# Kernel optimization log

Measured on AMD Instinct MI355X. Metric: run time of the kernel, lower is better.

The kernel has to match this reference:

```python
import jax, jax.numpy as jnp
import numpy as np

H = 1024      # hidden_size
NH = 16       # num heads
HD = H // NH  # head dim
B, S = 2, 2048


def setup_inputs() -> dict:
    key = jax.random.key(0)
    ks = jax.random.split(key, 10)
    s = 1.0 / np.sqrt(H)
    return {
        "hidden_states": jax.random.normal(ks[0], (B, S, H), dtype=jnp.float32),
        "attention_mask": jax.random.randint(ks[1], (B, S), 0, 2, dtype=jnp.int32),
        "Wq": jax.random.normal(ks[2], (H, H), dtype=jnp.float32) * s,
        "bq": jnp.zeros((H,), dtype=jnp.float32),
        "Wk": jax.random.normal(ks[3], (H, H), dtype=jnp.float32) * s,
        "bk": jnp.zeros((H,), dtype=jnp.float32),
        "Wv": jax.random.normal(ks[4], (H, H), dtype=jnp.float32) * s,
        "bv": jnp.zeros((H,), dtype=jnp.float32),
        "Wo": jax.random.normal(ks[5], (H, H), dtype=jnp.float32) * s,
        "bo": jnp.zeros((H,), dtype=jnp.float32),
    }


def _heads(x):
    # [B,S,H] -> [B,NH,S,HD]
    b, s, _ = x.shape
    return x.reshape(b, s, NH, HD).transpose(0, 2, 1, 3)


def reference(hidden_states, attention_mask, Wq, bq, Wk, bk, Wv, bv, Wo, bo):
    q = _heads(hidden_states @ Wq + bq)
    k = _heads(hidden_states @ Wk + bk)
    v = _heads(hidden_states @ Wv + bv)
    scores = jnp.einsum("bhqd,bhkd->bhqk", q, k) / jnp.sqrt(jnp.float32(HD))
    mask = attention_mask.astype(scores.dtype)[:, None, None, :]  # [B,1,1,S]
    scores = scores + mask * -10000.0
    probs = jax.nn.softmax(scores, axis=-1)  # dropout is identity in eval
    ctx = jnp.einsum("bhqk,bhkd->bhqd", probs, v)
    ctx = ctx.transpose(0, 2, 1, 3).reshape(hidden_states.shape[0], hidden_states.shape[1], H)
    return ctx @ Wo + bo
```

## Files before the change

kernel.cpp:

```cpp
#include <hip/hip_runtime.h>
#include <stdint.h>
#include <stddef.h>

#define S_LEN 2048
#define BATCH 2
#define HID 1024
#define NHEADS 16
#define HDIM 64

typedef __attribute__((ext_vector_type(8))) short short8;
typedef __attribute__((ext_vector_type(4))) short short4v;
typedef __attribute__((ext_vector_type(4))) float float4v;

#define MFMA32(a, b, c) __builtin_amdgcn_mfma_f32_16x16x32_bf16((a), (b), (c), 0, 0, 0)

#if __has_builtin(__builtin_amdgcn_mfma_f32_16x16x16_bf16)
#define MFMA16(a, b, c) __builtin_amdgcn_mfma_f32_16x16x16_bf16((a), (b), (c), 0, 0, 0)
#elif __has_builtin(__builtin_amdgcn_mfma_f32_16x16x16bf16_1k)
#define MFMA16(a, b, c) __builtin_amdgcn_mfma_f32_16x16x16bf16_1k((a), (b), (c), 0, 0, 0)
#else
static __device__ __forceinline__ float4v mfma16_asm(short4v a, short4v b, float4v c) {
  asm volatile("v_mfma_f32_16x16x16_bf16 %0, %1, %2, %0" : "+v"(c) : "v"(a), "v"(b));
  return c;
}
#define MFMA16(a, b, c) mfma16_asm((a), (b), (c))
#endif

#define SCALE_L2E 0.18033688011f

__device__ __forceinline__ short f2bf(float f) {
  union { float f; uint32_t u; } v; v.f = f;
  uint32_t u = v.u;
  uint32_t r = (u + 0x7fffu + ((u >> 16) & 1u)) >> 16;
  return (short)(uint16_t)r;
}

__device__ __forceinline__ short4v pack_bf16x4(float4v v) {
  union { short4v s; uint32_t u[2]; } U;
  U.u[0] = __builtin_amdgcn_perm(__float_as_uint(v[1]) + 0x8000u,
                                 __float_as_uint(v[0]) + 0x8000u, 0x07060302u);
  U.u[1] = __builtin_amdgcn_perm(__float_as_uint(v[3]) + 0x8000u,
                                 __float_as_uint(v[2]) + 0x8000u, 0x07060302u);
  return U.s;
}

__device__ __forceinline__ void gl_lds16(const void* g, void* l) {
  __builtin_amdgcn_global_load_lds((const __attribute__((address_space(1))) void*)g,
                                   (__attribute__((address_space(3))) void*)l,
                                   16, 0, 0);
}

__global__ __launch_bounds__(256) void prep_cast(const float* __restrict__ x,
                                                 short* __restrict__ xbf) {
  int gid = blockIdx.x * 256 + threadIdx.x;
  const float4v* src = (const float4v*)x;
  float4v v = src[gid];
  short4v o;
  o[0] = f2bf(v[0]); o[1] = f2bf(v[1]); o[2] = f2bf(v[2]); o[3] = f2bf(v[3]);
  ((short4v*)xbf)[gid] = o;
}

__global__ __launch_bounds__(256) void prep_idx(const int* __restrict__ mask,
                                                short* __restrict__ maskc,
                                                short* __restrict__ iidx,
                                                int* __restrict__ nkinfo) {
  __shared__ int sc[256];
  const int t = threadIdx.x;
  const short neg = f2bf(-14426.9504f);
  for (int b = 0; b < BATCH; b++) {
    int m[8]; int lc = 0;
    const int* mb = mask + b * S_LEN + t * 8;
#pragma unroll
    for (int j = 0; j < 8; j++) { m[j] = mb[j]; lc += (m[j] == 0); }
    sc[t] = lc;
    __syncthreads();
#pragma unroll
    for (int off = 1; off < 256; off <<= 1) {
      int u = (t >= off) ? sc[t - off] : 0;
      int v = sc[t];
      __syncthreads();
      sc[t] = u + v;
      __syncthreads();
    }
    int excl = sc[t] - lc;
    int nk = sc[255];
    if (t == 0) { nkinfo[b] = (nk + 63) & ~63; nkinfo[2 + b] = nk; }
    int run = excl;
#pragma unroll
    for (int j = 0; j < 8; j++) {
      if (m[j] == 0) { iidx[b * S_LEN + run] = (short)(t * 8 + j); run++; }
    }
    for (int i = t; i < S_LEN; i += 256)
      maskc[b * S_LEN + i] = (i < nk) ? (short)0 : neg;
    __syncthreads();
  }
}

__global__ __launch_bounds__(256) void prep_compact(const short* __restrict__ xbf,
                                                    const short* __restrict__ iidx,
                                                    const int* __restrict__ nkinfo,
                                                    short* __restrict__ xc) {
  const int t = threadIdx.x;
  const int b = blockIdx.x >> 8;
  const int row = (blockIdx.x & 255) * 8 + (t >> 5);
  const int ch = (t & 31) * 32;
  const int nk = nkinfo[2 + b];
  short* dst = xc + ((size_t)b * S_LEN + row) * HID + ch;
  if (row < nk) {
    const short* src = xbf + ((size_t)b * S_LEN + iidx[b * S_LEN + row]) * HID + ch;
#pragma unroll
    for (int k = 0; k < 4; k++) *(short8*)(dst + k * 8) = *(const short8*)(src + k * 8);
  } else {
#pragma unroll
    for (int k = 0; k < 4; k++) *(short8*)(dst + k * 8) = (short8)0;
  }
}

__global__ __launch_bounds__(256) void prep_transpose(const float* __restrict__ w0,
                                                      const float* __restrict__ w1,
                                                      const float* __restrict__ w2,
                                                      const float* __restrict__ w3,
                                                      short* __restrict__ wt) {
  __shared__ short lds[64 * 66];
  int z = blockIdx.z;
  const float* w = (z == 0) ? w0 : (z == 1) ? w1 : (z == 2) ? w2 : w3;
  short* out = wt + (size_t)z * HID * HID;
  int k0 = blockIdx.x * 64, n0 = blockIdx.y * 64;
  int lane = threadIdx.x & 63, wrp = threadIdx.x >> 6;
#pragma unroll
  for (int i = 0; i < 16; i++) {
    int rr = wrp + i * 4;
    lds[lane * 66 + rr] = f2bf(w[(size_t)(k0 + rr) * HID + n0 + lane]);
  }
  __syncthreads();
#pragma unroll
  for (int i = 0; i < 16; i++) {
    int nn = wrp + i * 4;
    out[(size_t)(n0 + nn) * HID + k0 + lane] = lds[nn * 66 + lane];
  }
}

#define VPS 136
template <int BM, int BN, bool TRANS_EP, bool DBUF>
__global__ __launch_bounds__(256) void gemm_bt(const short* __restrict__ A0,
                                               const short* __restrict__ AC,
                                               const short* __restrict__ WTbase,
                                               const float* __restrict__ bq,
                                               const float* __restrict__ bk,
                                               const float* __restrict__ bv,
                                               const float* __restrict__ bo,
                                               short* __restrict__ outQ,
                                               short* __restrict__ outK,
                                               short* __restrict__ outVt,
                                               float* __restrict__ outF,
                                               const int* __restrict__ nki,
                                               int mode_base) {
  constexpr int RI = BM / 32;
  constexpr int RJ = BN / 32;
  constexpr int TILE = BM * 128 + BN * 128;
  constexpr int LSZ1 = DBUF ? TILE * 2 : TILE;
  constexpr int LSZ = (TRANS_EP && LSZ1 < 128 * VPS * 2) ? 128 * VPS * 2 : LSZ1;
  __shared__ __align__(16) char lds[LSZ];
  const int tid = threadIdx.x;
  const int lane = tid & 63, w = tid >> 6;
  const int wm = w & 1, wn = w >> 1;
  const int quad = lane >> 4, l15 = lane & 15;
  const int mode = mode_base + blockIdx.z;
  const int m0 = blockIdx.x * BM, n0 = blockIdx.y * BN;
  if ((mode == 1 || mode == 2) && (m0 & 2047) >= nki[m0 >> 11]) return;
  const short* A = (mode == 1 || mode == 2) ? AC : A0;
  const short* Bt = WTbase + (size_t)mode * HID * HID;
  const float* bias = (mode == 0) ? bq : (mode == 1) ? bk : (mode == 2) ? bv : bo;

  float4v acc[RI][RJ];
#pragma unroll
  for (int i = 0; i < RI; i++)
#pragma unroll
    for (int j = 0; j < RJ; j++) acc[i][j] = (float4v)0.0f;

  auto issue = [&](int k0, char* buf) {
#pragma unroll
    for (int inst = 0; inst < BM / 32; inst++) {
      int p = inst * 256 + tid;
      int r = p >> 3;
      int c = (p & 7) ^ (r & 7);
      gl_lds16(A + (size_t)(m0 + r) * HID + k0 + c * 8, buf + p * 16);
    }
#pragma unroll
    for (int inst = 0; inst < BN / 32; inst++) {
      int p = inst * 256 + tid;
      int r = p >> 3;
      int c = (p & 7) ^ (r & 7);
      gl_lds16(Bt + (size_t)(n0 + r) * HID + k0 + c * 8, buf + BM * 128 + p * 16);
    }
  };

  auto compute = [&](const char* buf) {
#pragma unroll
    for (int kk = 0; kk < 2; kk++) {
      short8 af[RI], bf[RJ];
#pragma unroll
      for (int i = 0; i < RI; i++) {
        int ra = wm * (BM / 2) + i * 16 + l15;
        af[i] = *(const short8*)(buf + ra * 128 + (((kk * 4 + quad) ^ (ra & 7)) * 16));
      }
#pragma unroll
      for (int j = 0; j < RJ; j++) {
        int rb = wn * (BN / 2) + j * 16 + l15;
        bf[j] = *(const short8*)(buf + BM * 128 + rb * 128 + (((kk * 4 + quad) ^ (rb & 7)) * 16));
      }
#pragma unroll
      for (int i = 0; i < RI; i++)
#pragma unroll
        for (int j = 0; j < RJ; j++)
          acc[i][j] = MFMA32(af[i], bf[j], acc[i][j]);
    }
  };

  if (DBUF) {
    constexpr int NLD = BM / 32 + BN / 32;
    issue(0, lds);
#pragma unroll 1
    for (int t = 0; t < HID / 64; t++) {
      if (t < HID / 64 - 1) {
        issue((t + 1) * 64, lds + ((t + 1) & 1) * TILE);
        asm volatile("s_waitcnt vmcnt(%0)" ::"i"(NLD) : "memory");
      } else {
        asm volatile("s_waitcnt vmcnt(0)" ::: "memory");
      }
      __builtin_amdgcn_s_barrier();
      asm volatile("" ::: "memory");
      compute(lds + (t & 1) * TILE);
      asm volatile("" ::: "memory");
      __builtin_amdgcn_s_barrier();
    }
  } else {
    for (int k0 = 0; k0 < HID; k0 += 64) {
      __syncthreads();
      issue(k0, lds);
      __syncthreads();
      compute(lds);
    }
  }

  if (TRANS_EP && mode == 2) {
    short* eb = (short*)lds;
    __syncthreads();
#pragma unroll
    for (int j = 0; j < RJ; j++) {
      int nl = wn * (BN / 2) + j * 16 + l15;
      float bsv = bias[n0 + nl];
#pragma unroll
      for (int i = 0; i < RI; i++)
#pragma unroll
        for (int r = 0; r < 4; r++) {
          int ml = wm * (BM / 2) + i * 16 + quad * 4 + r;
          eb[nl * VPS + ml] = f2bf(acc[i][j][r] + bsv);
        }
    }
    __syncthreads();
    int row = tid >> 1, half = tid & 1;
    int n = n0 + row, h = n >> 6, d = n & 63;
    int b = m0 >> 11, sc = (m0 & 2047) + half * 64;
    short* dst = outVt + ((size_t)(b * NHEADS + h) * HDIM + d) * S_LEN + sc;
    const short* src = eb + row * VPS + half * 64;
#pragma unroll
    for (int c = 0; c < 8; c++)
      *(short8*)(dst + c * 8) = *(const short8*)(src + c * 8);
    return;
  }

#pragma unroll
  for (int i = 0; i < RI; i++) {
#pragma unroll
    for (int j = 0; j < RJ; j++) {
      int n = n0 + wn * (BN / 2) + j * 16 + l15;
      float bsv = bias[n];
#pragma unroll
      for (int r = 0; r < 4; r++) {
        int m = m0 + wm * (BM / 2) + i * 16 + quad * 4 + r;
        float val = acc[i][j][r] + bsv;
        if (mode == 3) {
          outF[(size_t)m * HID + n] = val;
        } else {
          int b = m >> 11, s = m & 2047, h = n >> 6, d = n & 63;
          if (mode == 1) val *= SCALE_L2E;
          short u = f2bf(val);
          if (mode == 0)
            outQ[((size_t)(b * NHEADS + h) * S_LEN + s) * HDIM + d] = u;
          else
            outK[((size_t)(b * NHEADS + h) * S_LEN + s) * HDIM + d] = u;
        }
      }
    }
  }
}

#define AT_DB 16384
#define AT_VOFF 8192
#define ALDS_M 32768

__device__ __forceinline__ float* buf_addr(float* base, int row, int col) {
  return base + row * 64 + ((((col >> 2) ^ (row & 15)) << 2) | (col & 3));
}

__global__ __launch_bounds__(256, 4) void attn(const short* __restrict__ Qb,
                                               const short* __restrict__ Kb,
                                               const short* __restrict__ Vt,
                                               const short* __restrict__ maskc,
                                               const int* __restrict__ nkinfo,
                                               short* __restrict__ ctx) {
  __shared__ __align__(16) char lds[36864];
  const int tid = threadIdx.x, lane = tid & 63, w = tid >> 6;
  const int quad = lane >> 4, l15 = lane & 15;
  const int qhalf = w & 1, khalf = w >> 1;
  const int h = blockIdx.y, b = blockIdx.z, bh = b * NHEADS + h;
  const short* Qh = Qb + (size_t)bh * S_LEN * HDIM;
  const short* Kh = Kb + (size_t)bh * S_LEN * HDIM;
  const short* Vh = Vt + (size_t)bh * HDIM * S_LEN;
  const short* mbase = maskc + b * S_LEN;
  const int qb0 = blockIdx.x * 64;
  const int nkp = nkinfo[b];

  auto issueKV = [&](int kb, int bufi) {
    char* base = lds + bufi * AT_DB;
#pragma unroll
    for (int inst = 0; inst < 2; inst++) {
      int p = inst * 256 + tid;
      int r = p >> 3, c = (p & 7) ^ (r & 7);
      gl_lds16(Kh + (size_t)(kb + r) * HDIM + c * 8, base + p * 16);
      gl_lds16(Vh + (size_t)r * S_LEN + kb + c * 8, base + AT_VOFF + p * 16);
    }
  };

  gl_lds16(mbase + tid * 8, lds + ALDS_M + tid * 16);
  issueKV(0, 0);

  short8 qf[2][2];
#pragma unroll
  for (int qt = 0; qt < 2; qt++)
#pragma unroll
    for (int kk = 0; kk < 2; kk++)
      qf[qt][kk] = *(const short8*)(Qh + (size_t)(qb0 + qhalf * 32 + qt * 16 + l15) * HDIM + kk * 32 + quad * 8);

  float4v o[2][4];
#pragma unroll
  for (int qt = 0; qt < 2; qt++)
#pragma unroll
    for (int nd = 0; nd < 4; nd++) o[qt][nd] = (float4v)0.0f;
  float lp[2] = {0.0f, 0.0f};

#pragma unroll 1
  for (int kb = 0; kb < nkp; kb += 64) {
    const int cur = (kb >> 6) & 1;
    const char* base = lds + cur * AT_DB;
    if (kb + 64 < nkp) {
      issueKV(kb + 64, cur ^ 1);
      asm volatile("s_waitcnt vmcnt(%0)" ::"i"(4) : "memory");
    } else {
      asm volatile("s_waitcnt vmcnt(0)" ::: "memory");
    }
    __builtin_amdgcn_s_barrier();
    asm volatile("" ::: "memory");

#pragma unroll
    for (int mt = 0; mt < 2; mt++) {
      short4v bvf[4];
      {
        int ch = khalf * 4 + mt * 2 + (quad >> 1);
        int sub = (quad & 1) * 8;
#pragma unroll
        for (int nd = 0; nd < 4; nd++) {
          int rv = nd * 16 + l15;
          bvf[nd] = *(const short4v*)(base + AT_VOFF + rv * 128 + ((ch ^ (rv & 7)) * 16) + sub);
        }
      }
      int rk = khalf * 32 + mt * 16 + l15;
      short8 ka0 = *(const short8*)(base + rk * 128 + ((quad ^ (rk & 7)) * 16));
      short8 ka1 = *(const short8*)(base + rk * 128 + (((4 + quad) ^ (rk & 7)) * 16));
      float4v mbv;
      {
        int midx = kb + khalf * 32 + mt * 16 + quad * 4;
        short4v ms = *(const short4v*)(lds + ALDS_M + midx * 2);
#pragma unroll
        for (int r = 0; r < 4; r++)
          mbv[r] = __uint_as_float(((uint32_t)(uint16_t)ms[r]) << 16);
      }
#pragma unroll
      for (int qt = 0; qt < 2; qt++) {
        float4v c = mbv;
        c = MFMA32(ka0, qf[qt][0], c);
        c = MFMA32(ka1, qf[qt][1], c);
        float4v ev;
#pragma unroll
        for (int r = 0; r < 4; r++) ev[r] = __builtin_amdgcn_exp2f(c[r]);
        lp[qt] += (ev[0] + ev[1]) + (ev[2] + ev[3]);
        short4v ap = pack_bf16x4(ev);
#pragma unroll
        for (int nd = 0; nd < 4; nd++) o[qt][nd] = MFMA16(ap, bvf[nd], o[qt][nd]);
      }
    }
    asm volatile("" ::: "memory");
    __builtin_amdgcn_s_barrier();
  }

#pragma unroll
  for (int qt = 0; qt < 2; qt++) {
    lp[qt] += __shfl_xor(lp[qt], 16, 64);
    lp[qt] += __shfl_xor(lp[qt], 32, 64);
  }
  float* lrowS = (float*)(lds + ALDS_M);
  float* bufP = (float*)(lds + qhalf * 8192);
  if (quad == 0) {
#pragma unroll
    for (int qt = 0; qt < 2; qt++) lrowS[w * 32 + qt * 16 + l15] = lp[qt];
  }
  if (khalf == 1) {
#pragma unroll
    for (int qt = 0; qt < 2; qt++)
#pragma unroll
      for (int nd = 0; nd < 4; nd++)
#pragma unroll
        for (int r = 0; r < 4; r++)
          *buf_addr(bufP, qt * 16 + quad * 4 + r, nd * 16 + l15) = o[qt][nd][r];
  }
  __syncthreads();
  if (khalf == 0) {
#pragma unroll
    for (int qt = 0; qt < 2; qt++)
#pragma unroll
      for (int nd = 0; nd < 4; nd++)
#pragma unroll
        for (int r = 0; r < 4; r++) {
          float* p = buf_addr(bufP, qt * 16 + quad * 4 + r, nd * 16 + l15);
          *p = *p + o[qt][nd][r];
        }
  }
  __syncthreads();
  int row = w * 16 + l15;
  float ls = lrowS[row] + lrowS[64 + row];
  float inv = 1.0f / ls;
  float* bufq = (float*)(lds + (row >> 5) * 8192);
  int brow = row & 31;
  short* dstp = ctx + ((size_t)(b * S_LEN + qb0 + row) * HID + h * HDIM + quad * 16);
#pragma unroll
  for (int half = 0; half < 2; half++) {
    int c0 = quad * 16 + half * 8;
    float4v x0 = *(float4v*)buf_addr(bufq, brow, c0);
    float4v x1 = *(float4v*)buf_addr(bufq, brow, c0 + 4);
    union { short8 s; short4v h[2]; } R;
    float4v s0, s1;
#pragma unroll
    for (int i = 0; i < 4; i++) { s0[i] = x0[i] * inv; s1[i] = x1[i] * inv; }
    R.h[0] = pack_bf16x4(s0);
    R.h[1] = pack_bf16x4(s1);
    *(short8*)(dstp + half * 8) = R.s;
  }
}

extern "C" void kernel_launch(void* const* d_in, const int* in_sizes, int n_in,
                              void* d_out, int out_size, void* d_ws, size_t ws_size,
                              hipStream_t stream) {
  const float* hs = (const float*)d_in[0];
  const int* mask = (const int*)d_in[1];
  const float* Wq = (const float*)d_in[2];
  const float* bq = (const float*)d_in[3];
  const float* Wk = (const float*)d_in[4];
  const float* bk = (const float*)d_in[5];
  const float* Wv = (const float*)d_in[6];
  const float* bv = (const float*)d_in[7];
  const float* Wo = (const float*)d_in[8];
  const float* bo = (const float*)d_in[9];
  float* out = (float*)d_out;
  char* ws = (char*)d_ws;

  short* XBF = (short*)(ws);
  short* CTX = (short*)(ws);
  short* WT  = (short*)(ws + (size_t)(8u << 20));
  short* QB  = (short*)(ws + (size_t)(16u << 20));
  short* KB  = (short*)(ws + (size_t)(24u << 20));
  short* VTt = (short*)(ws + (size_t)(32u << 20));
  short* MBc = (short*)(ws + (size_t)(40u << 20));
  short* IIDX = (short*)(ws + (size_t)(40u << 20) + (64u << 10));
  int*   NKI  = (int*)(ws + (size_t)(40u << 20) + (128u << 10));
  short* XC  = (short*)(ws + (size_t)(41u << 20));

  prep_cast<<<4096, 256, 0, stream>>>(hs, XBF);
  prep_idx<<<1, 256, 0, stream>>>(mask, MBc, IIDX, NKI);
  prep_compact<<<512, 256, 0, stream>>>(XBF, IIDX, NKI, XC);
  prep_transpose<<<dim3(16, 16, 4), 256, 0, stream>>>(Wq, Wk, Wv, Wo, WT);
  gemm_bt<128, 128, true, true><<<dim3(32, 8, 3), 256, 0, stream>>>(XBF, XC, WT, bq, bk, bv, bo, QB, KB, VTt, nullptr, NKI, 0);
  attn<<<dim3(32, NHEADS, BATCH), 256, 0, stream>>>(QB, KB, VTt, MBc, NKI, CTX);
  gemm_bt<64, 128, false, true><<<dim3(64, 8, 1), 256, 0, stream>>>(CTX, nullptr, WT, bq, bk, bv, bo, nullptr, nullptr, nullptr, out, nullptr, 3);
}
```

Baseline: 175.6 us.

## Merge prep kernels into one launch and gather K/V rows inside the GEMM

The cast, weight transpose and mask-index kernels are merged into a single prep_all launch that dispatches on block index. The separate compaction kernel and its XC buffer are removed. The QKV GEMM now gathers unmasked rows directly through per-thread precomputed source pointers from the index list, and padded index entries are set to zero. This saves kernel launches and a full copy of the activations, at the cost of non-contiguous row loads in the K/V GEMM and a single-block scan that runs alongside the other prep blocks.

```diff
diff --git a/kernel.cpp b/kernel.cpp
--- a/kernel.cpp
+++ b/kernel.cpp
@@ -50,22 +50,51 @@
                                    16, 0, 0);
 }
 
-__global__ __launch_bounds__(256) void prep_cast(const float* __restrict__ x,
-                                                 short* __restrict__ xbf) {
-  int gid = blockIdx.x * 256 + threadIdx.x;
-  const float4v* src = (const float4v*)x;
-  float4v v = src[gid];
-  short4v o;
-  o[0] = f2bf(v[0]); o[1] = f2bf(v[1]); o[2] = f2bf(v[2]); o[3] = f2bf(v[3]);
-  ((short4v*)xbf)[gid] = o;
-}
-
-__global__ __launch_bounds__(256) void prep_idx(const int* __restrict__ mask,
+__global__ __launch_bounds__(256) void prep_all(const float* __restrict__ x,
+                                                const int* __restrict__ mask,
+                                                const float* __restrict__ w0,
+                                                const float* __restrict__ w1,
+                                                const float* __restrict__ w2,
+                                                const float* __restrict__ w3,
+                                                short* __restrict__ xbf,
+                                                short* __restrict__ wt,
                                                 short* __restrict__ maskc,
                                                 short* __restrict__ iidx,
                                                 int* __restrict__ nkinfo) {
+  __shared__ short slds[64 * 66];
   __shared__ int sc[256];
-  const int t = threadIdx.x;
+  const int bid = blockIdx.x, t = threadIdx.x;
+
+  if (bid < 4096) {
+    int gid = bid * 256 + t;
+    float4v v = ((const float4v*)x)[gid];
+    short4v o;
+    o[0] = f2bf(v[0]); o[1] = f2bf(v[1]); o[2] = f2bf(v[2]); o[3] = f2bf(v[3]);
+    ((short4v*)xbf)[gid] = o;
+    return;
+  }
+
+  if (bid < 5120) {
+    int tt = bid - 4096;
+    int z = tt >> 8;
+    const float* w = (z == 0) ? w0 : (z == 1) ? w1 : (z == 2) ? w2 : w3;
+    short* out = wt + (size_t)z * HID * HID;
+    int k0 = (tt & 15) * 64, n0 = ((tt >> 4) & 15) * 64;
+    int lane = t & 63, wrp = t >> 6;
+#pragma unroll
+    for (int i = 0; i < 16; i++) {
+      int rr = wrp + i * 4;
+      slds[lane * 66 + rr] = f2bf(w[(size_t)(k0 + rr) * HID + n0 + lane]);
+    }
+    __syncthreads();
+#pragma unroll
+    for (int i = 0; i < 16; i++) {
+      int nn = wrp + i * 4;
+      out[(size_t)(n0 + nn) * HID + k0 + lane] = slds[nn * 66 + lane];
+    }
+    return;
+  }
+
   const short neg = f2bf(-14426.9504f);
   for (int b = 0; b < BATCH; b++) {
     int m[8]; int lc = 0;
@@ -90,60 +119,16 @@
     for (int j = 0; j < 8; j++) {
       if (m[j] == 0) { iidx[b * S_LEN + run] = (short)(t * 8 + j); run++; }
     }
+    for (int i = nk + t; i < S_LEN; i += 256) iidx[b * S_LEN + i] = 0;
     for (int i = t; i < S_LEN; i += 256)
       maskc[b * S_LEN + i] = (i < nk) ? (short)0 : neg;
     __syncthreads();
   }
 }
 
-__global__ __launch_bounds__(256) void prep_compact(const short* __restrict__ xbf,
-                                                    const short* __restrict__ iidx,
-                                                    const int* __restrict__ nkinfo,
-                                                    short* __restrict__ xc) {
-  const int t = threadIdx.x;
-  const int b = blockIdx.x >> 8;
-  const int row = (blockIdx.x & 255) * 8 + (t >> 5);
-  const int ch = (t & 31) * 32;
-  const int nk = nkinfo[2 + b];
-  short* dst = xc + ((size_t)b * S_LEN + row) * HID + ch;
-  if (row < nk) {
-    const short* src = xbf + ((size_t)b * S_LEN + iidx[b * S_LEN + row]) * HID + ch;
-#pragma unroll
-    for (int k = 0; k < 4; k++) *(short8*)(dst + k * 8) = *(const short8*)(src + k * 8);
-  } else {
-#pragma unroll
-    for (int k = 0; k < 4; k++) *(short8*)(dst + k * 8) = (short8)0;
-  }
-}
-
-__global__ __launch_bounds__(256) void prep_transpose(const float* __restrict__ w0,
-                                                      const float* __restrict__ w1,
-                                                      const float* __restrict__ w2,
-                                                      const float* __restrict__ w3,
-                                                      short* __restrict__ wt) {
-  __shared__ short lds[64 * 66];
-  int z = blockIdx.z;
-  const float* w = (z == 0) ? w0 : (z == 1) ? w1 : (z == 2) ? w2 : w3;
-  short* out = wt + (size_t)z * HID * HID;
-  int k0 = blockIdx.x * 64, n0 = blockIdx.y * 64;
-  int lane = threadIdx.x & 63, wrp = threadIdx.x >> 6;
-#pragma unroll
-  for (int i = 0; i < 16; i++) {
-    int rr = wrp + i * 4;
-    lds[lane * 66 + rr] = f2bf(w[(size_t)(k0 + rr) * HID + n0 + lane]);
-  }
-  __syncthreads();
-#pragma unroll
-  for (int i = 0; i < 16; i++) {
-    int nn = wrp + i * 4;
-    out[(size_t)(n0 + nn) * HID + k0 + lane] = lds[nn * 66 + lane];
-  }
-}
-
 #define VPS 136
 template <int BM, int BN, bool TRANS_EP, bool DBUF>
 __global__ __launch_bounds__(256) void gemm_bt(const short* __restrict__ A0,
-                                               const short* __restrict__ AC,
                                                const short* __restrict__ WTbase,
                                                const float* __restrict__ bq,
                                                const float* __restrict__ bk,
@@ -153,6 +138,7 @@
                                                short* __restrict__ outK,
                                                short* __restrict__ outVt,
                                                float* __restrict__ outF,
+                                               const short* __restrict__ iidx,
                                                const int* __restrict__ nki,
                                                int mode_base) {
   constexpr int RI = BM / 32;
@@ -167,11 +153,31 @@
   const int quad = lane >> 4, l15 = lane & 15;
   const int mode = mode_base + blockIdx.z;
   const int m0 = blockIdx.x * BM, n0 = blockIdx.y * BN;
-  if ((mode == 1 || mode == 2) && (m0 & 2047) >= nki[m0 >> 11]) return;
-  const short* A = (mode == 1 || mode == 2) ? AC : A0;
+  const bool gath = (mode == 1 || mode == 2);
+  if (gath && (m0 & 2047) >= nki[m0 >> 11]) return;
   const short* Bt = WTbase + (size_t)mode * HID * HID;
   const float* bias = (mode == 0) ? bq : (mode == 1) ? bk : (mode == 2) ? bv : bo;
 
+  const short* aptr[BM / 32];
+#pragma unroll
+  for (int inst = 0; inst < BM / 32; inst++) {
+    int p = inst * 256 + tid;
+    int r = p >> 3, c = (p & 7) ^ (r & 7);
+    int srow = m0 + r;
+    if (gath) {
+      int b = m0 >> 11;
+      srow = b * S_LEN + (int)iidx[b * S_LEN + (m0 & 2047) + r];
+    }
+    aptr[inst] = A0 + (size_t)srow * HID + c * 8;
+  }
+  const short* bptr[BN / 32];
+#pragma unroll
+  for (int inst = 0; inst < BN / 32; inst++) {
+    int p = inst * 256 + tid;
+    int r = p >> 3, c = (p & 7) ^ (r & 7);
+    bptr[inst] = Bt + (size_t)(n0 + r) * HID + c * 8;
+  }
+
   float4v acc[RI][RJ];
 #pragma unroll
   for (int i = 0; i < RI; i++)
@@ -182,16 +188,12 @@
 #pragma unroll
     for (int inst = 0; inst < BM / 32; inst++) {
       int p = inst * 256 + tid;
-      int r = p >> 3;
-      int c = (p & 7) ^ (r & 7);
-      gl_lds16(A + (size_t)(m0 + r) * HID + k0 + c * 8, buf + p * 16);
+      gl_lds16(aptr[inst] + k0, buf + p * 16);
     }
 #pragma unroll
     for (int inst = 0; inst < BN / 32; inst++) {
       int p = inst * 256 + tid;
-      int r = p >> 3;
-      int c = (p & 7) ^ (r & 7);
-      gl_lds16(Bt + (size_t)(n0 + r) * HID + k0 + c * 8, buf + BM * 128 + p * 16);
+      gl_lds16(bptr[inst] + k0, buf + BM * 128 + p * 16);
     }
   };
 
@@ -483,13 +485,9 @@
   short* MBc = (short*)(ws + (size_t)(40u << 20));
   short* IIDX = (short*)(ws + (size_t)(40u << 20) + (64u << 10));
   int*   NKI  = (int*)(ws + (size_t)(40u << 20) + (128u << 10));
-  short* XC  = (short*)(ws + (size_t)(41u << 20));
-
-  prep_cast<<<4096, 256, 0, stream>>>(hs, XBF);
-  prep_idx<<<1, 256, 0, stream>>>(mask, MBc, IIDX, NKI);
-  prep_compact<<<512, 256, 0, stream>>>(XBF, IIDX, NKI, XC);
-  prep_transpose<<<dim3(16, 16, 4), 256, 0, stream>>>(Wq, Wk, Wv, Wo, WT);
-  gemm_bt<128, 128, true, true><<<dim3(32, 8, 3), 256, 0, stream>>>(XBF, XC, WT, bq, bk, bv, bo, QB, KB, VTt, nullptr, NKI, 0);
+
+  prep_all<<<5121, 256, 0, stream>>>(hs, mask, Wq, Wk, Wv, Wo, XBF, WT, MBc, IIDX, NKI);
+  gemm_bt<128, 128, true, true><<<dim3(32, 8, 3), 256, 0, stream>>>(XBF, WT, bq, bk, bv, bo, QB, KB, VTt, nullptr, IIDX, NKI, 0);
   attn<<<dim3(32, NHEADS, BATCH), 256, 0, stream>>>(QB, KB, VTt, MBc, NKI, CTX);
-  gemm_bt<64, 128, false, true><<<dim3(64, 8, 1), 256, 0, stream>>>(CTX, nullptr, WT, bq, bk, bv, bo, nullptr, nullptr, nullptr, out, nullptr, 3);
-}
+  gemm_bt<64, 128, false, true><<<dim3(64, 8, 1), 256, 0, stream>>>(CTX, WT, bq, bk, bv, bo, nullptr, nullptr, nullptr, out, nullptr, nullptr, 3);
+}
```

After: 170.9 us. -2.7%, faster.
